# Performance work log

Hardware: AMD Instinct MI355X
Metric: run time of the kernel (lower is better)

The kernel has to match this reference:

```python
import jax, jax.numpy as jnp
import numpy as np
from jax import lax

GROUP = 8
EPS = 1e-5

def _bn_relu(x, gamma, beta):
    # BatchNorm3d in train mode: batch stats over (N,D,H,W) per channel, then ReLU
    mean = x.mean(axis=(0, 2, 3, 4), keepdims=True)
    var = x.var(axis=(0, 2, 3, 4), keepdims=True)
    xn = (x - mean) * lax.rsqrt(var + EPS)
    return jax.nn.relu(xn * gamma[None, :, None, None, None] + beta[None, :, None, None, None])

def _group_norm(x, gamma, beta):
    # GroupNorm(cg, cg): one channel per group -> per (n,c) normalization over spatial dims
    mean = x.mean(axis=(2, 3, 4), keepdims=True)
    var = x.var(axis=(2, 3, 4), keepdims=True)
    xn = (x - mean) * lax.rsqrt(var + EPS)
    return xn * gamma[None, :, None, None, None] + beta[None, :, None, None, None]

def setup_inputs() -> dict:
    key = jax.random.key(0)
    ks = jax.random.split(key, 4)
    b, c, d, h, w = 2, 64, 64, 64, 64
    cg = c // GROUP
    return {
        "x": jax.random.normal(ks[0], (b, c, d, h, w), dtype=jnp.float32),
        "conv1_w": jax.random.normal(ks[1], (cg, cg, 1, 1, 1), dtype=jnp.float32) * 0.1,
        "conv1_b": jnp.zeros((cg,), jnp.float32),
        "bn1_g": jnp.ones((cg,), jnp.float32),
        "bn1_b": jnp.zeros((cg,), jnp.float32),
        "conv3_w": jax.random.normal(ks[2], (cg, cg, 3, 3, 3), dtype=jnp.float32) * 0.05,
        "conv3_b": jnp.zeros((cg,), jnp.float32),
        "bn3_g": jnp.ones((cg,), jnp.float32),
        "bn3_b": jnp.zeros((cg,), jnp.float32),
        "gn_g": jnp.ones((cg,), jnp.float32),
        "gn_b": jnp.zeros((cg,), jnp.float32),
    }

def reference(x, conv1_w, conv1_b, bn1_g, bn1_b, conv3_w, conv3_b, bn3_g, bn3_b, gn_g, gn_b):
    b, c, d, h, w = x.shape
    g = GROUP
    cg = c // g
    gx = x.reshape(b * g, cg, d, h, w)

    # directional average pools -> all stacked along axis 2 as length-(d+h+w) profiles
    x_h = gx.mean(axis=(3, 4), keepdims=True)                      # (bg,cg,d,1,1)
    x_w = gx.mean(axis=(2, 4), keepdims=True).transpose(0, 1, 3, 2, 4)  # (bg,cg,h,1,1)
    x_d = gx.mean(axis=(2, 3), keepdims=True).transpose(0, 1, 4, 3, 2)  # (bg,cg,w,1,1)
    cat = jnp.concatenate([x_h, x_w, x_d], axis=2)                 # (bg,cg,d+h+w,1,1)

    # 1x1x1 conv == channel mix, then BN+ReLU
    hwd = jnp.einsum('oi,bisuv->bosuv', conv1_w[:, :, 0, 0, 0], cat) + conv1_b[None, :, None, None, None]
    hwd = _bn_relu(hwd, bn1_g, bn1_b)

    a_h = jax.nn.sigmoid(hwd[:, :, :d]).reshape(b * g, cg, d, 1, 1)
    a_w = jax.nn.sigmoid(hwd[:, :, d:d + h]).reshape(b * g, cg, 1, h, 1)
    a_d = jax.nn.sigmoid(hwd[:, :, d + h:]).reshape(b * g, cg, 1, 1, w)

    x1 = _group_norm(gx * (a_h * a_w * a_d), gn_g, gn_b)           # (bg,cg,d,h,w)

    x2 = lax.conv_general_dilated(gx, conv3_w, (1, 1, 1), 'SAME',
                                  dimension_numbers=('NCDHW', 'OIDHW', 'NCDHW'))
    x2 = _bn_relu(x2 + conv3_b[None, :, None, None, None], bn3_g, bn3_b)

    x11 = jax.nn.softmax(x1.mean(axis=(2, 3, 4)), axis=-1)         # (bg,cg)
    x21 = jax.nn.softmax(x2.mean(axis=(2, 3, 4)), axis=-1)         # (bg,cg)
    x12 = x1.reshape(b * g, cg, d * h * w)
    x22 = x2.reshape(b * g, cg, d * h * w)

    weights = (jnp.einsum('bc,bcn->bn', x11, x22) +
               jnp.einsum('bc,bcn->bn', x21, x12)).reshape(b * g, 1, d, h, w)
    return (gx * jax.nn.sigmoid(weights)).reshape(b, c, d, h, w)
```

## Files before the change

### kernel.cpp

```cpp
#include <hip/hip_runtime.h>
#include <math.h>
#include <stdint.h>

#define VOL 262144
#define EPSF 1e-5f

typedef _Float16 half4_t __attribute__((ext_vector_type(4)));
typedef _Float16 half8 __attribute__((ext_vector_type(8)));
typedef float floatx4 __attribute__((ext_vector_type(4)));

__device__ __forceinline__ float waveReduceSum(float v) {
    #pragma unroll
    for (int off = 32; off > 0; off >>= 1) v += __shfl_down(v, off);
    return v;
}

__device__ __forceinline__ uint32_t pk2(float a, float b) {
    uint32_t r;
    asm("v_cvt_pkrtz_f16_f32 %0, %1, %2" : "=v"(r) : "v"(a), "v"(b));
    return r;
}

__global__ void k_wprep(const float* __restrict__ w3, _Float16* __restrict__ wB) {
    int i = blockIdx.x * 256 + threadIdx.x;
    if (i < 3584) {
        int j = i & 7;
        int lane = (i >> 3) & 63;
        int ks = i >> 9;
        int oc = lane & 15;
        int t = ks * 4 + (lane >> 4);
        float v = 0.f;
        if (oc < 8 && t < 27) v = w3[(oc * 8 + j) * 27 + t];
        wB[i] = (_Float16)v;
    }
}

__global__ void k_pools(const float* __restrict__ x, float* __restrict__ catS) {
    int r = blockIdx.x >> 4, p4 = blockIdx.x & 15;
    const float* base = x + (size_t)r * VOL + ((size_t)(p4 * 4) << 12);
    __shared__ float sd[4], sh[64], sw[64];
    int tid = threadIdx.x;
    if (tid < 4) sd[tid] = 0.f;
    if (tid < 64) { sh[tid] = 0.f; sw[tid] = 0.f; }
    __syncthreads();
    int w4 = (tid & 15) * 4;
    int hr = tid >> 4;
    int lane = tid & 63;
    float dacc[4] = {0.f, 0.f, 0.f, 0.f};
    float hacc[4] = {0.f, 0.f, 0.f, 0.f};
    float wacc[4] = {0.f, 0.f, 0.f, 0.f};
    #pragma unroll
    for (int p = 0; p < 4; p++) {
        const float* pd = base + (p << 12);
        #pragma unroll
        for (int j = 0; j < 4; j++) {
            float4 v = *(const float4*)(pd + ((hr + j * 16) << 6) + w4);
            float s = v.x + v.y + v.z + v.w;
            dacc[p] += s; hacc[j] += s;
            wacc[0] += v.x; wacc[1] += v.y; wacc[2] += v.z; wacc[3] += v.w;
        }
    }
    #pragma unroll
    for (int p = 0; p < 4; p++) {
        float s = waveReduceSum(dacc[p]);
        if (lane == 0) atomicAdd(&sd[p], s);
    }
    #pragma unroll
    for (int j = 0; j < 4; j++) {
        float hv = hacc[j];
        hv += __shfl_xor(hv, 1); hv += __shfl_xor(hv, 2);
        hv += __shfl_xor(hv, 4); hv += __shfl_xor(hv, 8);
        if ((lane & 15) == 0) atomicAdd(&sh[hr + j * 16], hv);
    }
    #pragma unroll
    for (int k = 0; k < 4; k++) {
        float wv = wacc[k];
        wv += __shfl_xor(wv, 16); wv += __shfl_xor(wv, 32);
        if (lane < 16) atomicAdd(&sw[w4 + k], wv);
    }
    __syncthreads();
    float* o = catS + (size_t)r * 192;
    if (tid < 4)                       atomicAdd(&o[p4 * 4 + tid], sd[tid]);
    else if (tid >= 64 && tid < 128)   atomicAdd(&o[64 + tid - 64], sh[tid - 64]);
    else if (tid >= 128 && tid < 192)  atomicAdd(&o[128 + tid - 128], sw[tid - 128]);
}

__global__ void k_attn_stats(const float* __restrict__ catS, const float* __restrict__ w1,
                             const float* __restrict__ b1, const float* __restrict__ g1,
                             const float* __restrict__ be1, float* __restrict__ attnp) {
    __shared__ float r1[256], r2[256];
    __shared__ float wsm[64];
    int tid = threadIdx.x;
    if (tid < 64) wsm[tid] = w1[tid] * (1.f / 4096.f);
    __syncthreads();
    int o = tid >> 5, j = tid & 31;
    float s1 = 0.f, s2 = 0.f;
    for (int idx = j; idx < 3072; idx += 32) {
        int bgI = idx / 192, s = idx - bgI * 192;
        const float* cp = catS + (size_t)bgI * 1536 + s;
        float h = b1[o];
        #pragma unroll
        for (int i = 0; i < 8; i++) h += wsm[o * 8 + i] * cp[i * 192];
        s1 += h; s2 += h * h;
    }
    r1[tid] = s1; r2[tid] = s2;
    __syncthreads();
    for (int st = 16; st > 0; st >>= 1) {
        if (j < st) { r1[tid] += r1[tid + st]; r2[tid] += r2[tid + st]; }
        __syncthreads();
    }
    if (j == 0) {
        float mean = r1[tid] / 3072.f;
        float var  = r2[tid] / 3072.f - mean * mean;
        float sc = g1[o] * rsqrtf(var + EPSF);
        attnp[o] = sc; attnp[8 + o] = be1[o] - mean * sc;
    }
}

__global__ void k_attn_apply(const float* __restrict__ catS, const float* __restrict__ w1,
                             const float* __restrict__ b1, const float* __restrict__ attnp,
                             float* __restrict__ aout) {
    __shared__ float wsm[64];
    int tid = threadIdx.x;
    if (tid < 64) wsm[tid] = w1[tid] * (1.f / 4096.f);
    __syncthreads();
    int e = blockIdx.x * 256 + tid;
    int bgI = e / 1536;
    int rem = e - bgI * 1536;
    int oo = rem / 192;
    int s = rem - oo * 192;
    const float* cp = catS + (size_t)bgI * 1536 + s;
    float h = b1[oo];
    #pragma unroll
    for (int i = 0; i < 8; i++) h += wsm[oo * 8 + i] * cp[i * 192];
    float v = attnp[oo] * h + attnp[8 + oo];
    v = fmaxf(v, 0.f);
    aout[e] = 1.f / (1.f + __expf(-v));
}

#define SLICE_B (18 * 66 * 16)

__device__ __forceinline__ void stage_slice(const float* __restrict__ xb, int dd,
                                            char* smem, int slot, int h0, int tid,
                                            const float* __restrict__ sA, int d0,
                                            float* g1, float* g2) {
    char* sb = smem + slot * SLICE_B;
    bool dok = (dd >= 0) && (dd < 64);
    bool core = (dd >= d0) && (dd < d0 + 8);
    const float* pd = xb + ((size_t)(dd & 63) << 12);
    for (int u = tid; u < 288; u += 256) {
        int hl = u >> 4;
        int w4 = (u & 15) << 2;
        int gh = h0 - 1 + hl;
        bool ok = dok && (gh >= 0) && (gh < 64);
        bool acc = core && (hl >= 1) && (hl <= 16);
        float vv[8][4];
        #pragma unroll
        for (int ic = 0; ic < 8; ic++) {
            float4 t = make_float4(0.f, 0.f, 0.f, 0.f);
            if (ok) t = *(const float4*)(pd + ((size_t)ic << 18) + (gh << 6) + w4);
            vv[ic][0] = t.x; vv[ic][1] = t.y; vv[ic][2] = t.z; vv[ic][3] = t.w;
        }
        if (acc) {
            #pragma unroll
            for (int ic = 0; ic < 8; ic++) {
                const float* Ap = sA + ic * 192;
                float ad = Ap[dd] * Ap[64 + gh];
                float y0 = vv[ic][0] * ad * Ap[128 + w4];
                float y1 = vv[ic][1] * ad * Ap[128 + w4 + 1];
                float y2 = vv[ic][2] * ad * Ap[128 + w4 + 2];
                float y3 = vv[ic][3] * ad * Ap[128 + w4 + 3];
                g1[ic] += y0 + y1 + y2 + y3;
                g2[ic] += y0 * y0 + y1 * y1 + y2 * y2 + y3 * y3;
            }
        }
        char* wp = sb + ((hl * 66) + 1 + w4) * 16;
        #pragma unroll
        for (int j = 0; j < 4; j++) {
            uint4 q;
            q.x = pk2(vv[0][j], vv[1][j]);
            q.y = pk2(vv[2][j], vv[3][j]);
            q.z = pk2(vv[4][j], vv[5][j]);
            q.w = pk2(vv[6][j], vv[7][j]);
            *(uint4*)(wp + j * 16) = q;
        }
    }
}

__global__ __launch_bounds__(256) void k_conv(const float* __restrict__ x,
                                              const _Float16* __restrict__ wB,
                                              const float* __restrict__ b3,
                                              const float* __restrict__ a,
                                              _Float16* __restrict__ x2h,
                                              float* __restrict__ stats,
                                              float* __restrict__ gs) {
    __shared__ __align__(16) char smem[3 * SLICE_B + 768 + 6144];
    float* wred = (float*)(smem + 3 * SLICE_B);
    float* wgn  = wred + 128;
    float* sA   = (float*)(smem + 3 * SLICE_B + 768);
    int blk = blockIdx.x;
    int bg = blk >> 5;
    int rem = blk & 31;
    int ht = rem >> 3;
    int dc = rem & 7;
    int h0 = ht << 4;
    int d0 = dc << 3;
    int tid = threadIdx.x;
    int lane = tid & 63, wid = tid >> 6;
    int lm = lane & 15, lg = lane >> 4;
    const float* xb = x + ((size_t)bg << 21);

    half8 bfr[7];
    #pragma unroll
    for (int ks = 0; ks < 7; ks++)
        bfr[ks] = *(const half8*)(wB + (ks << 9) + (lane << 3));

    float b3v = (lm < 8) ? b3[lm] : 0.f;

    int rel[7], kzv[7];
    #pragma unroll
    for (int ks = 0; ks < 7; ks++) {
        int t = ks * 4 + lg; if (t > 26) t = 26;
        int kz = t / 9, r9 = t - kz * 9;
        int ky = r9 / 3, kx = r9 - ky * 3;
        kzv[ks] = kz;
        rel[ks] = (((ky + wid * 4) * 66) + kx + lm) << 4;
    }

    for (int u = tid; u < 108; u += 256) {
        int s = u / 36, r2 = u - s * 36;
        int hh = r2 >> 1, side = r2 & 1;
        uint4 z; z.x = 0; z.y = 0; z.z = 0; z.w = 0;
        *(uint4*)(smem + s * SLICE_B + ((hh * 66) + side * 65) * 16) = z;
    }
    for (int i = tid; i < 1536; i += 256) sA[i] = a[(size_t)bg * 1536 + i];
    __syncthreads();

    size_t eb = (((size_t)(bg * 8 + lm)) << 18) + ((size_t)(h0 + wid * 4) << 6) + (lg << 2);
    bool ocok = lm < 8;
    float ps = 0.f, pq = 0.f;
    float g1[8] = {0.f, 0.f, 0.f, 0.f, 0.f, 0.f, 0.f, 0.f};
    float g2[8] = {0.f, 0.f, 0.f, 0.f, 0.f, 0.f, 0.f, 0.f};

    stage_slice(xb, d0 - 1, smem, (d0 + 2) % 3, h0, tid, sA, d0, g1, g2);
    stage_slice(xb, d0,     smem, d0 % 3,       h0, tid, sA, d0, g1, g2);
    __syncthreads();

    for (int i = 0; i < 8; i++) {
        int d = d0 + i;
        stage_slice(xb, d + 1, smem, (d + 1) % 3, h0, tid, sA, d0, g1, g2);
        __syncthreads();
        int u0 = ((d + 2) % 3) * SLICE_B;
        int u1 = (d % 3) * SLICE_B;
        int u2 = ((d + 1) % 3) * SLICE_B;
        int ab[7];
        #pragma unroll
        for (int ks = 0; ks < 7; ks++)
            ab[ks] = (kzv[ks] == 0 ? u0 : (kzv[ks] == 1 ? u1 : u2)) + rel[ks];
        #pragma unroll
        for (int ri = 0; ri < 4; ri++) {
            #pragma unroll
            for (int wt = 0; wt < 4; wt++) {
                floatx4 acc = {b3v, b3v, b3v, b3v};
                #pragma unroll
                for (int ks = 0; ks < 7; ks++) {
                    half8 af = *(const half8*)(smem + ab[ks] + ((ri * 66 + wt * 16) << 4));
                    acc = __builtin_amdgcn_mfma_f32_16x16x32_f16(af, bfr[ks], acc, 0, 0, 0);
                }
                uint32_t q0 = pk2(acc[0], acc[1]);
                uint32_t q1 = pk2(acc[2], acc[3]);
                if (ocok) {
                    uint2 st; st.x = q0; st.y = q1;
                    *(uint2*)(x2h + eb + ((size_t)d << 12) + (ri << 6) + (wt << 4)) = st;
                }
                ps += acc[0] + acc[1] + acc[2] + acc[3];
                pq += acc[0] * acc[0] + acc[1] * acc[1] + acc[2] * acc[2] + acc[3] * acc[3];
            }
        }
        __syncthreads();
    }

    ps += __shfl_xor(ps, 16); ps += __shfl_xor(ps, 32);
    pq += __shfl_xor(pq, 16); pq += __shfl_xor(pq, 32);
    if (lane < 16) { wred[wid * 32 + lm] = ps; wred[wid * 32 + 16 + lm] = pq; }
    #pragma unroll
    for (int ic = 0; ic < 8; ic++) {
        float r1v = waveReduceSum(g1[ic]);
        float r2v = waveReduceSum(g2[ic]);
        if (lane == 0) { wgn[wid * 16 + ic] = r1v; wgn[wid * 16 + 8 + ic] = r2v; }
    }
    __syncthreads();
    if (tid < 8) {
        float t1 = wred[tid] + wred[32 + tid] + wred[64 + tid] + wred[96 + tid];
        float t2 = wred[16 + tid] + wred[48 + tid] + wred[80 + tid] + wred[112 + tid];
        atomicAdd(&stats[tid], t1);
        atomicAdd(&stats[8 + tid], t2);
        float q1 = wgn[tid] + wgn[16 + tid] + wgn[32 + tid] + wgn[48 + tid];
        float q2 = wgn[8 + tid] + wgn[24 + tid] + wgn[40 + tid] + wgn[56 + tid];
        atomicAdd(&gs[bg * 8 + tid], q1);
        atomicAdd(&gs[128 + bg * 8 + tid], q2);
    }
}

__global__ void k_finalize(const float* __restrict__ stats, const float* __restrict__ g3,
                           const float* __restrict__ be3, const float* __restrict__ gnb,
                           float* __restrict__ bnp, float* __restrict__ x11) {
    int tid = threadIdx.x;
    if (tid < 8) {
        float N = 16.f * (float)VOL;
        float mean = stats[tid] / N;
        float var  = stats[8 + tid] / N - mean * mean;
        float sc = g3[tid] * rsqrtf(var + EPSF);
        bnp[tid] = sc; bnp[8 + tid] = be3[tid] - mean * sc;
    }
    if (tid == 0) {
        float m = -1e30f;
        for (int c = 0; c < 8; c++) m = fmaxf(m, gnb[c]);
        float e[8], sum = 0.f;
        for (int c = 0; c < 8; c++) { e[c] = __expf(gnb[c] - m); sum += e[c]; }
        for (int c = 0; c < 8; c++) x11[c] = e[c] / sum;
    }
}

__global__ void k_relumean(const _Float16* __restrict__ x2h, const float* __restrict__ bnp,
                           float* __restrict__ mrelu) {
    int blk = blockIdx.x;
    int r = blk >> 3, part = blk & 7;
    int cc = r & 7;
    float sc = bnp[cc], sh = bnp[8 + cc];
    const half4_t* p = (const half4_t*)(x2h + (size_t)r * VOL + (size_t)part * 32768);
    int tid = threadIdx.x;
    float s = 0.f;
    for (int it = 0; it < 32; it++) {
        half4_t v = p[it * 256 + tid];
        s += fmaxf(sc * (float)v.x + sh, 0.f) + fmaxf(sc * (float)v.y + sh, 0.f)
           + fmaxf(sc * (float)v.z + sh, 0.f) + fmaxf(sc * (float)v.w + sh, 0.f);
    }
    s = waveReduceSum(s);
    __shared__ float wred[4];
    int lane = tid & 63, wid = tid >> 6;
    if (lane == 0) wred[wid] = s;
    __syncthreads();
    if (tid == 0) atomicAdd(&mrelu[r], wred[0] + wred[1] + wred[2] + wred[3]);
}

__global__ void k_soft21(const float* __restrict__ mrelu, float* __restrict__ x21) {
    int bg = threadIdx.x;
    if (bg < 16) {
        float v[8], m = -1e30f;
        for (int c = 0; c < 8; c++) { v[c] = mrelu[bg * 8 + c] / (float)VOL; m = fmaxf(m, v[c]); }
        float sum = 0.f;
        for (int c = 0; c < 8; c++) { v[c] = __expf(v[c] - m); sum += v[c]; }
        for (int c = 0; c < 8; c++) x21[bg * 8 + c] = v[c] / sum;
    }
}

__global__ void k_final(const float* __restrict__ x, const _Float16* __restrict__ x2h,
                        const float* __restrict__ a, const float* __restrict__ bnp,
                        const float* __restrict__ x11g, const float* __restrict__ x21g,
                        const float* __restrict__ gs, const float* __restrict__ gng,
                        const float* __restrict__ gnb, float* __restrict__ out) {
    int bg = blockIdx.x >> 8;
    int seg = blockIdx.x & 255;
    int tid = threadIdx.x;
    __shared__ float sa[1536];
    __shared__ float sc_[8], sh_[8], sx11[8], sx21[8], sgsc[8], sgsh[8];
    const float* ap = a + (size_t)bg * 1536;
    for (int i = tid; i < 1536; i += 256) sa[i] = ap[i];
    if (tid < 8) {
        int r = bg * 8 + tid;
        sc_[tid] = bnp[tid]; sh_[tid] = bnp[8 + tid];
        sx11[tid] = x11g[tid]; sx21[tid] = x21g[r];
        float mean = gs[r] / (float)VOL;
        float var  = gs[128 + r] / (float)VOL - mean * mean;
        float gr = rsqrtf(var + EPSF) * gng[tid];
        sgsc[tid] = gr; sgsh[tid] = gnb[tid] - mean * gr;
    }
    __syncthreads();
    int n = (seg * 256 + tid) * 4;
    int d = n >> 12, h = (n >> 6) & 63, w = n & 63;
    size_t base = ((size_t)bg << 21) + n;
    float4 xr[8];
    float w0 = 0.f, w1 = 0.f, w2 = 0.f, w3 = 0.f;
    #pragma unroll
    for (int c = 0; c < 8; c++) {
        size_t idx = base + ((size_t)c << 18);
        float4 xv = *(const float4*)(x + idx);
        half4_t v2 = *(const half4_t*)(x2h + idx);
        xr[c] = xv;
        float adh = sa[c * 192 + d] * sa[c * 192 + 64 + h] * sgsc[c];
        float x22_0 = fmaxf(sc_[c] * (float)v2.x + sh_[c], 0.f);
        float x22_1 = fmaxf(sc_[c] * (float)v2.y + sh_[c], 0.f);
        float x22_2 = fmaxf(sc_[c] * (float)v2.z + sh_[c], 0.f);
        float x22_3 = fmaxf(sc_[c] * (float)v2.w + sh_[c], 0.f);
        float x12_0 = xv.x * (adh * sa[c * 192 + 128 + w])     + sgsh[c];
        float x12_1 = xv.y * (adh * sa[c * 192 + 128 + w + 1]) + sgsh[c];
        float x12_2 = xv.z * (adh * sa[c * 192 + 128 + w + 2]) + sgsh[c];
        float x12_3 = xv.w * (adh * sa[c * 192 + 128 + w + 3]) + sgsh[c];
        w0 += sx11[c] * x22_0 + sx21[c] * x12_0;
        w1 += sx11[c] * x22_1 + sx21[c] * x12_1;
        w2 += sx11[c] * x22_2 + sx21[c] * x12_2;
        w3 += sx11[c] * x22_3 + sx21[c] * x12_3;
    }
    float s0 = 1.f / (1.f + __expf(-w0));
    float s1 = 1.f / (1.f + __expf(-w1));
    float s2 = 1.f / (1.f + __expf(-w2));
    float s3 = 1.f / (1.f + __expf(-w3));
    #pragma unroll
    for (int c = 0; c < 8; c++) {
        float4 o;
        o.x = xr[c].x * s0; o.y = xr[c].y * s1; o.z = xr[c].z * s2; o.w = xr[c].w * s3;
        *(float4*)(out + base + ((size_t)c << 18)) = o;
    }
}

extern "C" void kernel_launch(void* const* d_in, const int* in_sizes, int n_in,
                              void* d_out, int out_size, void* d_ws, size_t ws_size,
                              hipStream_t stream) {
    const float* x   = (const float*)d_in[0];
    const float* w1  = (const float*)d_in[1];
    const float* b1  = (const float*)d_in[2];
    const float* g1  = (const float*)d_in[3];
    const float* be1 = (const float*)d_in[4];
    const float* w3  = (const float*)d_in[5];
    const float* b3  = (const float*)d_in[6];
    const float* g3  = (const float*)d_in[7];
    const float* be3 = (const float*)d_in[8];
    const float* gng = (const float*)d_in[9];
    const float* gnb = (const float*)d_in[10];
    float* out = (float*)d_out;

    float* wsf       = (float*)d_ws;
    _Float16* x2h    = (_Float16*)d_ws;
    float* catS   = wsf + 16777216;
    float* stats  = catS + 24576;
    float* gs     = stats + 16;
    float* mrelu  = gs + 256;
    float* a      = mrelu + 128;
    float* bnp    = a + 24576;
    float* x11    = bnp + 16;
    float* x21    = x11 + 8;
    float* attnp  = x21 + 128;
    _Float16* wB  = (_Float16*)(attnp + 16);

    hipMemsetAsync(catS, 0, (24576 + 16 + 256 + 128) * sizeof(float), stream);

    k_wprep     <<<14, 256, 0, stream>>>(w3, wB);
    k_pools     <<<2048, 256, 0, stream>>>(x, catS);
    k_attn_stats<<<1, 256, 0, stream>>>(catS, w1, b1, g1, be1, attnp);
    k_attn_apply<<<96, 256, 0, stream>>>(catS, w1, b1, attnp, a);
    k_conv      <<<512, 256, 0, stream>>>(x, wB, b3, a, x2h, stats, gs);
    k_finalize  <<<1, 64, 0, stream>>>(stats, g3, be3, gnb, bnp, x11);
    k_relumean  <<<1024, 256, 0, stream>>>(x2h, bnp, mrelu);
    k_soft21    <<<1, 64, 0, stream>>>(mrelu, x21);
    k_final     <<<4096, 256, 0, stream>>>(x, x2h, a, bnp, x11, x21, gs, gng, gnb, out);
}
```

Measured before the change: 430.9 us.

## Prefetch next depth slice into registers during MFMA compute; pad LDS row stride

Global loads for slice d+2 are issued into registers before the MFMA loop for slice d. They are committed to the LDS ring buffer after a barrier, so memory latency overlaps tensor compute. The LDS row stride is padded from 66 to 67 entries to reduce bank conflicts on the fragment reads. The prefetch holds many extra live registers across the compute loop, which risks lower occupancy or spills, and adds a second barrier per iteration.

```diff
diff --git a/kernel.cpp b/kernel.cpp
--- a/kernel.cpp
+++ b/kernel.cpp
@@ -138,12 +138,13 @@
     aout[e] = 1.f / (1.f + __expf(-v));
 }
 
-#define SLICE_B (18 * 66 * 16)
-
-__device__ __forceinline__ void stage_slice(const float* __restrict__ xb, int dd,
-                                            char* smem, int slot, int h0, int tid,
-                                            const float* __restrict__ sA, int d0,
-                                            float* g1, float* g2) {
+#define WSTRIDE 67
+#define SLICE_B (18 * WSTRIDE * 16)
+
+__device__ __forceinline__ void stage_direct(const float* __restrict__ xb, int dd,
+                                             char* smem, int slot, int h0, int tid,
+                                             const float* __restrict__ sA, int d0,
+                                             float* g1, float* g2) {
     char* sb = smem + slot * SLICE_B;
     bool dok = (dd >= 0) && (dd < 64);
     bool core = (dd >= d0) && (dd < d0 + 8);
@@ -174,7 +175,7 @@
                 g2[ic] += y0 * y0 + y1 * y1 + y2 * y2 + y3 * y3;
             }
         }
-        char* wp = sb + ((hl * 66) + 1 + w4) * 16;
+        char* wp = sb + ((hl * WSTRIDE) + 1 + w4) * 16;
         #pragma unroll
         for (int j = 0; j < 4; j++) {
             uint4 q;
@@ -184,6 +185,35 @@
             q.w = pk2(vv[6][j], vv[7][j]);
             *(uint4*)(wp + j * 16) = q;
         }
+    }
+}
+
+__device__ __forceinline__ void commit_item(const float vv[8][4], int hl, int w4, int gh,
+                                            bool acc, char* sb,
+                                            const float* __restrict__ sA, int dd,
+                                            float* g1, float* g2) {
+    if (acc) {
+        #pragma unroll
+        for (int ic = 0; ic < 8; ic++) {
+            const float* Ap = sA + ic * 192;
+            float ad = Ap[dd] * Ap[64 + gh];
+            float y0 = vv[ic][0] * ad * Ap[128 + w4];
+            float y1 = vv[ic][1] * ad * Ap[128 + w4 + 1];
+            float y2 = vv[ic][2] * ad * Ap[128 + w4 + 2];
+            float y3 = vv[ic][3] * ad * Ap[128 + w4 + 3];
+            g1[ic] += y0 + y1 + y2 + y3;
+            g2[ic] += y0 * y0 + y1 * y1 + y2 * y2 + y3 * y3;
+        }
+    }
+    char* wp = sb + ((hl * WSTRIDE) + 1 + w4) * 16;
+    #pragma unroll
+    for (int j = 0; j < 4; j++) {
+        uint4 q;
+        q.x = pk2(vv[0][j], vv[1][j]);
+        q.y = pk2(vv[2][j], vv[3][j]);
+        q.z = pk2(vv[4][j], vv[5][j]);
+        q.w = pk2(vv[6][j], vv[7][j]);
+        *(uint4*)(wp + j * 16) = q;
     }
 }
 
@@ -224,14 +254,14 @@
         int kz = t / 9, r9 = t - kz * 9;
         int ky = r9 / 3, kx = r9 - ky * 3;
         kzv[ks] = kz;
-        rel[ks] = (((ky + wid * 4) * 66) + kx + lm) << 4;
+        rel[ks] = (((ky + wid * 4) * WSTRIDE) + kx + lm) << 4;
     }
 
     for (int u = tid; u < 108; u += 256) {
         int s = u / 36, r2 = u - s * 36;
         int hh = r2 >> 1, side = r2 & 1;
         uint4 z; z.x = 0; z.y = 0; z.z = 0; z.w = 0;
-        *(uint4*)(smem + s * SLICE_B + ((hh * 66) + side * 65) * 16) = z;
+        *(uint4*)(smem + s * SLICE_B + ((hh * WSTRIDE) + side * 65) * 16) = z;
     }
     for (int i = tid; i < 1536; i += 256) sA[i] = a[(size_t)bg * 1536 + i];
     __syncthreads();
@@ -242,14 +272,43 @@
     float g1[8] = {0.f, 0.f, 0.f, 0.f, 0.f, 0.f, 0.f, 0.f};
     float g2[8] = {0.f, 0.f, 0.f, 0.f, 0.f, 0.f, 0.f, 0.f};
 
-    stage_slice(xb, d0 - 1, smem, (d0 + 2) % 3, h0, tid, sA, d0, g1, g2);
-    stage_slice(xb, d0,     smem, d0 % 3,       h0, tid, sA, d0, g1, g2);
-    __syncthreads();
+    stage_direct(xb, d0 - 1, smem, (d0 + 2) % 3, h0, tid, sA, d0, g1, g2);
+    stage_direct(xb, d0,     smem, d0 % 3,       h0, tid, sA, d0, g1, g2);
+    stage_direct(xb, d0 + 1, smem, (d0 + 1) % 3, h0, tid, sA, d0, g1, g2);
+    __syncthreads();
+
+    int hl0 = tid >> 4,        w40 = (tid & 15) << 2,  gh0 = h0 - 1 + hl0;
+    int hl1 = 16 + (tid >> 4), w41 = w40,              gh1 = h0 - 1 + hl1;
+    bool it1 = tid < 32;
 
     for (int i = 0; i < 8; i++) {
         int d = d0 + i;
-        stage_slice(xb, d + 1, smem, (d + 1) % 3, h0, tid, sA, d0, g1, g2);
-        __syncthreads();
+        float vv0[8][4], vv1[8][4];
+        int dd = d + 2;
+        bool core, acc0 = false, acc1 = false;
+        if (i < 7) {
+            bool dok = dd < 64;
+            core = (dd < d0 + 8);
+            const float* pd = xb + ((size_t)(dd & 63) << 12);
+            bool ok0 = dok && (gh0 >= 0) && (gh0 < 64);
+            acc0 = core && (hl0 >= 1);
+            #pragma unroll
+            for (int ic = 0; ic < 8; ic++) {
+                float4 t = make_float4(0.f, 0.f, 0.f, 0.f);
+                if (ok0) t = *(const float4*)(pd + ((size_t)ic << 18) + (gh0 << 6) + w40);
+                vv0[ic][0] = t.x; vv0[ic][1] = t.y; vv0[ic][2] = t.z; vv0[ic][3] = t.w;
+            }
+            if (it1) {
+                bool ok1 = dok && (gh1 < 64);
+                acc1 = core && (hl1 <= 16);
+                #pragma unroll
+                for (int ic = 0; ic < 8; ic++) {
+                    float4 t = make_float4(0.f, 0.f, 0.f, 0.f);
+                    if (ok1) t = *(const float4*)(pd + ((size_t)ic << 18) + (gh1 << 6) + w41);
+                    vv1[ic][0] = t.x; vv1[ic][1] = t.y; vv1[ic][2] = t.z; vv1[ic][3] = t.w;
+                }
+            }
+        }
         int u0 = ((d + 2) % 3) * SLICE_B;
         int u1 = (d % 3) * SLICE_B;
         int u2 = ((d + 1) % 3) * SLICE_B;
@@ -264,7 +323,7 @@
                 floatx4 acc = {b3v, b3v, b3v, b3v};
                 #pragma unroll
                 for (int ks = 0; ks < 7; ks++) {
-                    half8 af = *(const half8*)(smem + ab[ks] + ((ri * 66 + wt * 16) << 4));
+                    half8 af = *(const half8*)(smem + ab[ks] + ((ri * WSTRIDE + wt * 16) << 4));
                     acc = __builtin_amdgcn_mfma_f32_16x16x32_f16(af, bfr[ks], acc, 0, 0, 0);
                 }
                 uint32_t q0 = pk2(acc[0], acc[1]);
@@ -276,6 +335,12 @@
                 ps += acc[0] + acc[1] + acc[2] + acc[3];
                 pq += acc[0] * acc[0] + acc[1] * acc[1] + acc[2] * acc[2] + acc[3] * acc[3];
             }
+        }
+        __syncthreads();
+        if (i < 7) {
+            char* sb = smem + ((d + 2) % 3) * SLICE_B;
+            commit_item(vv0, hl0, w40, gh0, acc0, sb, sA, dd, g1, g2);
+            if (it1) commit_item(vv1, hl1, w41, gh1, acc1, sb, sA, dd, g1, g2);
         }
         __syncthreads();
     }
```

New measurement: 445.9 us. 3.5% more time.

## Pad conv slice stride and hoist attention factors into registers

Applied to the files above, without the earlier changes.

Changes the LDS row stride of the staged fp16 slices from 66 to 67 entries, which moves rows onto different LDS banks when the MFMA operands are read. It drops the per-block shared copy of the attention vector and its sync, and instead preloads each thread's fixed h and w attention factors into registers once, reading the d factor from global memory per slice. The staging loop is unrolled into one fixed item per thread plus a second item for the first 32 threads. This raises register pressure (about 48 extra floats per thread) and adds a small scattered global read on every slice.

```diff
diff --git a/kernel.cpp b/kernel.cpp
--- a/kernel.cpp
+++ b/kernel.cpp
@@ -138,52 +138,76 @@
     aout[e] = 1.f / (1.f + __expf(-v));
 }
 
-#define SLICE_B (18 * 66 * 16)
+#define WSTRIDE 67
+#define SLICE_B (18 * WSTRIDE * 16)
+
+__device__ __forceinline__ void stage_item(const float* __restrict__ pd, bool ok, bool acc,
+                                           int hl, int w4, int gh, char* sb,
+                                           const float* __restrict__ ad,
+                                           const float* __restrict__ Ah,
+                                           const float (*__restrict__ Aw)[4],
+                                           float* g1, float* g2) {
+    float vv[8][4];
+    #pragma unroll
+    for (int ic = 0; ic < 8; ic++) {
+        float4 t = make_float4(0.f, 0.f, 0.f, 0.f);
+        if (ok) t = *(const float4*)(pd + ((size_t)ic << 18) + (gh << 6) + w4);
+        vv[ic][0] = t.x; vv[ic][1] = t.y; vv[ic][2] = t.z; vv[ic][3] = t.w;
+    }
+    if (acc) {
+        #pragma unroll
+        for (int ic = 0; ic < 8; ic++) {
+            float adh = ad[ic] * Ah[ic];
+            float y0 = vv[ic][0] * adh * Aw[ic][0];
+            float y1 = vv[ic][1] * adh * Aw[ic][1];
+            float y2 = vv[ic][2] * adh * Aw[ic][2];
+            float y3 = vv[ic][3] * adh * Aw[ic][3];
+            g1[ic] += y0 + y1 + y2 + y3;
+            g2[ic] += y0 * y0 + y1 * y1 + y2 * y2 + y3 * y3;
+        }
+    }
+    char* wp = sb + ((hl * WSTRIDE) + 1 + w4) * 16;
+    #pragma unroll
+    for (int j = 0; j < 4; j++) {
+        uint4 q;
+        q.x = pk2(vv[0][j], vv[1][j]);
+        q.y = pk2(vv[2][j], vv[3][j]);
+        q.z = pk2(vv[4][j], vv[5][j]);
+        q.w = pk2(vv[6][j], vv[7][j]);
+        *(uint4*)(wp + j * 16) = q;
+    }
+}
 
 __device__ __forceinline__ void stage_slice(const float* __restrict__ xb, int dd,
                                             char* smem, int slot, int h0, int tid,
-                                            const float* __restrict__ sA, int d0,
-                                            float* g1, float* g2) {
+                                            const float* __restrict__ aG, int d0,
+                                            float* g1, float* g2,
+                                            const float* __restrict__ Ah0,
+                                            const float* __restrict__ Ah1,
+                                            const float (*__restrict__ Aw)[4]) {
     char* sb = smem + slot * SLICE_B;
     bool dok = (dd >= 0) && (dd < 64);
     bool core = (dd >= d0) && (dd < d0 + 8);
     const float* pd = xb + ((size_t)(dd & 63) << 12);
-    for (int u = tid; u < 288; u += 256) {
-        int hl = u >> 4;
-        int w4 = (u & 15) << 2;
-        int gh = h0 - 1 + hl;
-        bool ok = dok && (gh >= 0) && (gh < 64);
-        bool acc = core && (hl >= 1) && (hl <= 16);
-        float vv[8][4];
-        #pragma unroll
-        for (int ic = 0; ic < 8; ic++) {
-            float4 t = make_float4(0.f, 0.f, 0.f, 0.f);
-            if (ok) t = *(const float4*)(pd + ((size_t)ic << 18) + (gh << 6) + w4);
-            vv[ic][0] = t.x; vv[ic][1] = t.y; vv[ic][2] = t.z; vv[ic][3] = t.w;
-        }
-        if (acc) {
-            #pragma unroll
-            for (int ic = 0; ic < 8; ic++) {
-                const float* Ap = sA + ic * 192;
-                float ad = Ap[dd] * Ap[64 + gh];
-                float y0 = vv[ic][0] * ad * Ap[128 + w4];
-                float y1 = vv[ic][1] * ad * Ap[128 + w4 + 1];
-                float y2 = vv[ic][2] * ad * Ap[128 + w4 + 2];
-                float y3 = vv[ic][3] * ad * Ap[128 + w4 + 3];
-                g1[ic] += y0 + y1 + y2 + y3;
-                g2[ic] += y0 * y0 + y1 * y1 + y2 * y2 + y3 * y3;
-            }
-        }
-        char* wp = sb + ((hl * 66) + 1 + w4) * 16;
-        #pragma unroll
-        for (int j = 0; j < 4; j++) {
-            uint4 q;
-            q.x = pk2(vv[0][j], vv[1][j]);
-            q.y = pk2(vv[2][j], vv[3][j]);
-            q.z = pk2(vv[4][j], vv[5][j]);
-            q.w = pk2(vv[6][j], vv[7][j]);
-            *(uint4*)(wp + j * 16) = q;
-        }
+    float ad[8];
+    if (core) {
+        #pragma unroll
+        for (int ic = 0; ic < 8; ic++) ad[ic] = aG[ic * 192 + dd];
+    } else {
+        #pragma unroll
+        for (int ic = 0; ic < 8; ic++) ad[ic] = 0.f;
+    }
+    int hl0 = tid >> 4, w4 = (tid & 15) << 2;
+    int gh0 = h0 - 1 + hl0;
+    bool ok0 = dok && (gh0 >= 0);
+    bool acc0 = core && (hl0 >= 1);
+    stage_item(pd, ok0, acc0, hl0, w4, gh0, sb, ad, Ah0, Aw, g1, g2);
+    if (tid < 32) {
+        int hl1 = 16 + (tid >> 4);
+        int gh1 = h0 - 1 + hl1;
+        bool ok1 = dok && (gh1 < 64);
+        bool acc1 = core && (hl1 <= 16);
+        stage_item(pd, ok1, acc1, hl1, w4, gh1, sb, ad, Ah1, Aw, g1, g2);
     }
 }
 
@@ -194,10 +218,9 @@
                                               _Float16* __restrict__ x2h,
                                               float* __restrict__ stats,
                                               float* __restrict__ gs) {
-    __shared__ __align__(16) char smem[3 * SLICE_B + 768 + 6144];
+    __shared__ __align__(16) char smem[3 * SLICE_B + 768];
     float* wred = (float*)(smem + 3 * SLICE_B);
     float* wgn  = wred + 128;
-    float* sA   = (float*)(smem + 3 * SLICE_B + 768);
     int blk = blockIdx.x;
     int bg = blk >> 5;
     int rem = blk & 31;
@@ -209,6 +232,7 @@
     int lane = tid & 63, wid = tid >> 6;
     int lm = lane & 15, lg = lane >> 4;
     const float* xb = x + ((size_t)bg << 21);
+    const float* aG = a + (size_t)bg * 1536;
 
     half8 bfr[7];
     #pragma unroll
@@ -216,6 +240,18 @@
         bfr[ks] = *(const half8*)(wB + (ks << 9) + (lane << 3));
 
     float b3v = (lm < 8) ? b3[lm] : 0.f;
+
+    int phl0 = tid >> 4, pw4 = (tid & 15) << 2;
+    int pgh0 = h0 - 1 + phl0;
+    int pgh1 = h0 + 15 + (tid >> 4);
+    float Ah0[8], Ah1[8], Aw[8][4];
+    #pragma unroll
+    for (int ic = 0; ic < 8; ic++) {
+        Ah0[ic] = (pgh0 >= 0) ? aG[ic * 192 + 64 + pgh0] : 0.f;
+        Ah1[ic] = (pgh1 < 64) ? aG[ic * 192 + 64 + pgh1] : 0.f;
+        #pragma unroll
+        for (int k = 0; k < 4; k++) Aw[ic][k] = aG[ic * 192 + 128 + pw4 + k];
+    }
 
     int rel[7], kzv[7];
     #pragma unroll
@@ -224,17 +260,15 @@
         int kz = t / 9, r9 = t - kz * 9;
         int ky = r9 / 3, kx = r9 - ky * 3;
         kzv[ks] = kz;
-        rel[ks] = (((ky + wid * 4) * 66) + kx + lm) << 4;
+        rel[ks] = (((ky + wid * 4) * WSTRIDE) + kx + lm) << 4;
     }
 
     for (int u = tid; u < 108; u += 256) {
         int s = u / 36, r2 = u - s * 36;
         int hh = r2 >> 1, side = r2 & 1;
         uint4 z; z.x = 0; z.y = 0; z.z = 0; z.w = 0;
-        *(uint4*)(smem + s * SLICE_B + ((hh * 66) + side * 65) * 16) = z;
-    }
-    for (int i = tid; i < 1536; i += 256) sA[i] = a[(size_t)bg * 1536 + i];
-    __syncthreads();
+        *(uint4*)(smem + s * SLICE_B + ((hh * WSTRIDE) + side * 65) * 16) = z;
+    }
 
     size_t eb = (((size_t)(bg * 8 + lm)) << 18) + ((size_t)(h0 + wid * 4) << 6) + (lg << 2);
     bool ocok = lm < 8;
@@ -242,13 +276,13 @@
     float g1[8] = {0.f, 0.f, 0.f, 0.f, 0.f, 0.f, 0.f, 0.f};
     float g2[8] = {0.f, 0.f, 0.f, 0.f, 0.f, 0.f, 0.f, 0.f};
 
-    stage_slice(xb, d0 - 1, smem, (d0 + 2) % 3, h0, tid, sA, d0, g1, g2);
-    stage_slice(xb, d0,     smem, d0 % 3,       h0, tid, sA, d0, g1, g2);
+    stage_slice(xb, d0 - 1, smem, (d0 + 2) % 3, h0, tid, aG, d0, g1, g2, Ah0, Ah1, Aw);
+    stage_slice(xb, d0,     smem, d0 % 3,       h0, tid, aG, d0, g1, g2, Ah0, Ah1, Aw);
     __syncthreads();
 
     for (int i = 0; i < 8; i++) {
         int d = d0 + i;
-        stage_slice(xb, d + 1, smem, (d + 1) % 3, h0, tid, sA, d0, g1, g2);
+        stage_slice(xb, d + 1, smem, (d + 1) % 3, h0, tid, aG, d0, g1, g2, Ah0, Ah1, Aw);
         __syncthreads();
         int u0 = ((d + 2) % 3) * SLICE_B;
         int u1 = (d % 3) * SLICE_B;
@@ -264,7 +298,7 @@
                 floatx4 acc = {b3v, b3v, b3v, b3v};
                 #pragma unroll
                 for (int ks = 0; ks < 7; ks++) {
-                    half8 af = *(const half8*)(smem + ab[ks] + ((ri * 66 + wt * 16) << 4));
+                    half8 af = *(const half8*)(smem + ab[ks] + ((ri * WSTRIDE + wt * 16) << 4));
                     acc = __builtin_amdgcn_mfma_f32_16x16x32_f16(af, bfr[ks], acc, 0, 0, 0);
                 }
                 uint32_t q0 = pk2(acc[0], acc[1]);
```

Measured after the change: 479.2 us. 11.2% more time.
